# Kernel optimization log

Hardware: AMD Instinct MI355X
Metric: run time of the kernel (lower is better)

The kernel has to match this reference:

```python
import jax, jax.numpy as jnp
import numpy as np

NUM_NODES = 100000
NUM_EDGES = 1200000
IN_CH = 64
HID_CH = 64
NUM_REL = 8
DEG = NUM_EDGES // NUM_NODES  # uniform degree 12


def setup_inputs() -> dict:
    key = jax.random.key(0)
    k1, k2, k3, k4 = jax.random.split(key, 4)
    x = jax.random.normal(k1, (NUM_NODES, IN_CH), dtype=jnp.float32)
    linear = jax.random.normal(k2, (NUM_REL, IN_CH, HID_CH), dtype=jnp.float32) * (1.0 / np.sqrt(IN_CH))
    ptr = jnp.arange(NUM_NODES + 1, dtype=jnp.int64) * DEG  # CSR row pointers, uniform degree
    idx = jax.random.randint(k3, (NUM_EDGES,), 0, NUM_NODES, dtype=jnp.int64)
    edge_types = jax.random.randint(k4, (NUM_EDGES,), 0, NUM_REL, dtype=jnp.int64)
    return {"x": x, "linear": linear, "ptr": ptr, "idx": idx,
            "edge_types": edge_types, "num_node": NUM_NODES}


def reference(x, linear, ptr, idx, edge_types, num_node):
    # Gather source-node features per edge: [E, in]
    gathered = x[idx]
    # Per-edge-type linear transform (loop over small fixed num_rel, like RGCNOP)
    out_e = jnp.zeros((gathered.shape[0], linear.shape[-1]), dtype=gathered.dtype)
    for r in range(linear.shape[0]):
        mask = (edge_types == r).astype(gathered.dtype)[:, None]
        out_e = out_e + mask * (gathered @ linear[r])
    # CSR scatter-sum aggregation over destination segments defined by ptr
    num_edges = idx.shape[0]
    seg_ids = jnp.searchsorted(ptr, jnp.arange(num_edges, dtype=ptr.dtype), side='right') - 1
    agg = jax.ops.segment_sum(out_e, seg_ids, num_segments=num_node)
    # Degree normalization
    deg = (ptr[1:] - ptr[:-1]).astype(agg.dtype)
    return agg / deg[:, None]
```

## Files before the change

kernel.cpp:

```cpp
#include <hip/hip_runtime.h>
#include <hip/hip_bf16.h>


#define THREADS 512
#define NPB 64
#define KDIM 512
#define LDA 520
#define MAXE 1024
#define WFRAG (4 * 16 * 64 * 8)

typedef __attribute__((ext_vector_type(8))) short bf16x8;
typedef __attribute__((ext_vector_type(4))) float f32x4;

extern __shared__ __align__(16) char smem[];

__device__ __forceinline__ unsigned short f2bf(float f) {
  __hip_bfloat16 h = __float2bfloat16(f);
  return *reinterpret_cast<unsigned short*>(&h);
}

__global__ __launch_bounds__(256) void pack_w(const void* __restrict__ wv,
                                              unsigned short* __restrict__ wsB) {
  const int lane = threadIdx.x & 63;
  const unsigned word = ((const unsigned*)wv)[lane];
  const int exf = (int)((word >> 7) & 0xFFu);
  const bool w_bf16 = __popcll(__ballot(exf >= 96 && exf < 160)) >= 48;
  for (int i = blockIdx.x * 256 + threadIdx.x; i < WFRAG; i += gridDim.x * 256) {
    const int j  = i & 7;
    const int l  = (i >> 3) & 63;
    const int kt = (i >> 9) & 15;
    const int nt = i >> 13;
    const int k  = kt * 32 + (l >> 4) * 8 + j;
    const int n  = nt * 16 + (l & 15);
    float v;
    if (w_bf16) v = __bfloat162float(((const __hip_bfloat16*)wv)[k * 64 + n]);
    else        v = ((const float*)wv)[k * 64 + n];
    wsB[i] = f2bf(v);
  }
}

#define ACC_SW(accrow, r, vv)                                        \
  switch (r) {                                                       \
    case 0: accrow[0] += (vv); break; case 1: accrow[1] += (vv); break; \
    case 2: accrow[2] += (vv); break; case 3: accrow[3] += (vv); break; \
    case 4: accrow[4] += (vv); break; case 5: accrow[5] += (vv); break; \
    case 6: accrow[6] += (vv); break; default: accrow[7] += (vv); break; }

__global__ __launch_bounds__(THREADS, 2)
void rgcn_fused(const void* __restrict__ xv,
                const void* __restrict__ wv,
                const int* __restrict__ p32,
                const int* __restrict__ i32,
                const int* __restrict__ t32,
                const unsigned short* __restrict__ wsB,
                float* __restrict__ out,
                int num_nodes) {
  __hip_bfloat16* aggS = (__hip_bfloat16*)smem;
  __hip_bfloat16* wtS  = aggS + NPB * LDA;
  char* tail = smem + (size_t)NPB * LDA * 2 + (wsB ? 0 : (size_t)64 * LDA * 2);
  float*    invS  = (float*)tail;
  int*      ptrS  = (int*)(tail + 256);
  unsigned* eMeta = (unsigned*)(tail + 256 + 272);

  const int tid   = threadIdx.x;
  const int lane  = tid & 63;
  const int wvid  = tid >> 6;
  const int node0 = blockIdx.x * NPB;

  const unsigned xword = ((const unsigned*)xv)[lane];
  const int exf = (int)((xword >> 7) & 0xFFu);
  const bool x_bf16 = __popcll(__ballot(exf >= 96 && exf < 160)) >= 48;
  const bool idx64 = (p32[1] == 0);

  auto ldptr = [&](int n) -> int { return idx64 ? p32[2 * n] : p32[n]; };

  const int ntop   = min(node0 + NPB, num_nodes);
  const int e_lo   = ldptr(node0);
  const int ecount = ldptr(ntop) - e_lo;
  const bool staged = (ecount > 0 && ecount <= MAXE);

  for (int i = tid; i <= NPB; i += THREADS)
    ptrS[i] = ldptr(min(node0 + i, num_nodes));

  if (staged) {
    for (int e = tid; e < ecount; e += THREADS) {
      const int ge = e_lo + e;
      const unsigned s = (unsigned)(idx64 ? i32[2 * ge] : i32[ge]);
      const unsigned r = (unsigned)(idx64 ? t32[2 * ge] : t32[ge]);
      eMeta[e] = s | (r << 24);
    }
  }

  if (!wsB) {
    if (x_bf16) {
      const __hip_bfloat16* wb = (const __hip_bfloat16*)wv;
      for (int i = tid; i < KDIM * 64; i += THREADS)
        wtS[(i & 63) * LDA + (i >> 6)] = wb[i];
    } else {
      const float* wf = (const float*)wv;
      for (int i = tid; i < KDIM * 64; i += THREADS)
        wtS[(i & 63) * LDA + (i >> 6)] = __float2bfloat16(wf[i]);
    }
  }

  __syncthreads();

  for (int i = tid; i < NPB; i += THREADS) {
    const int d = ptrS[i + 1] - ptrS[i];
    invS[i] = (d > 0 && node0 + i < num_nodes) ? 1.0f / (float)d : 0.0f;
  }

  if (staged && tid < NPB) {
    const int e0 = ptrS[tid] - e_lo;
    if (ptrS[tid + 1] - ptrS[tid] == 12) {
      unsigned a[12];
#pragma unroll
      for (int j = 0; j < 12; ++j) a[j] = eMeta[e0 + j];
#pragma unroll
      for (int r = 0; r < 12; ++r)
#pragma unroll
        for (int i = (r & 1); i + 1 < 12; i += 2) {
          const unsigned lo = min(a[i], a[i + 1]);
          const unsigned hi = max(a[i], a[i + 1]);
          a[i] = lo; a[i + 1] = hi;
        }
#pragma unroll
      for (int j = 0; j < 12; ++j) eMeta[e0 + j] = a[j];
    }
  }

  __syncthreads();

  const int c16 = lane & 15;
  const int qd  = lane >> 4;

  auto gather = [&](auto xp, auto loadrow) {
#pragma unroll
    for (int g = 0; g < 2; ++g) {
      const int nlb = wvid * 8 + g * 4;
      const int eq0 = ptrS[nlb + qd] - e_lo;
      const int dq  = ptrS[nlb + qd + 1] - e_lo - eq0;
      const bool okfast = staged && (node0 + nlb + 3 < num_nodes) &&
                          (__ballot(dq == 12) == ~0ull);
      if (okfast) {
        unsigned m[12];
#pragma unroll
        for (int j = 0; j < 12; ++j) m[j] = eMeta[eq0 + j];
        float4 v[12];
#pragma unroll
        for (int j = 0; j < 12; ++j)
          v[j] = loadrow((int)(m[j] & 0x00FFFFFFu), c16);
        __builtin_amdgcn_sched_barrier(0);

        unsigned short* dst0 =
            (unsigned short*)(aggS + (nlb + qd) * LDA) + 4 * c16;
        const ushort4 z4 = {0, 0, 0, 0};
#pragma unroll
        for (int r = 0; r < 8; ++r) *(ushort4*)(dst0 + r * 64) = z4;

        float4 cur = make_float4(0.f, 0.f, 0.f, 0.f);
        unsigned prev = 0xFFFFFFFFu;
#pragma unroll
        for (int j = 0; j < 12; ++j) {
          const unsigned rj = m[j] >> 24;
          const float mk = (rj == prev) ? 1.0f : 0.0f;
          cur.x = fmaf(cur.x, mk, v[j].x);
          cur.y = fmaf(cur.y, mk, v[j].y);
          cur.z = fmaf(cur.z, mk, v[j].z);
          cur.w = fmaf(cur.w, mk, v[j].w);
          ushort4 b;
          b.x = f2bf(cur.x); b.y = f2bf(cur.y);
          b.z = f2bf(cur.z); b.w = f2bf(cur.w);
          *(ushort4*)(dst0 + rj * 64) = b;
          prev = rj;
        }
      } else {
#pragma unroll
        for (int t = 0; t < 4; ++t) {
          const int nl = nlb + t;
          float a[8] = {0.f, 0.f, 0.f, 0.f, 0.f, 0.f, 0.f, 0.f};
          if (node0 + nl < num_nodes) {
            const int e0 = ptrS[nl] - e_lo, e1 = ptrS[nl + 1] - e_lo;
            for (int e = e0; e < e1; ++e) {
              unsigned mm;
              if (staged) mm = eMeta[e];
              else {
                const int ge = e_lo + e;
                mm = (unsigned)(idx64 ? i32[2 * ge] : i32[ge]) |
                     ((unsigned)(idx64 ? t32[2 * ge] : t32[ge]) << 24);
              }
              const float vv = (float)xp[(size_t)(mm & 0x00FFFFFFu) * 64 + lane];
              const int r = __builtin_amdgcn_readfirstlane((int)(mm >> 24));
              ACC_SW(a, r, vv)
            }
          }
#pragma unroll
          for (int r = 0; r < 8; ++r)
            aggS[nl * LDA + r * 64 + lane] = __float2bfloat16(a[r]);
        }
      }
    }
  };

  if (x_bf16) {
    const __hip_bfloat16* xb = (const __hip_bfloat16*)xv;
    auto lr = [&](int src, int c) -> float4 {
      const ushort4 u = ((const ushort4*)xv)[src * 16 + c];
      float4 f;
      f.x = __uint_as_float((unsigned)(unsigned short)u.x << 16);
      f.y = __uint_as_float((unsigned)(unsigned short)u.y << 16);
      f.z = __uint_as_float((unsigned)(unsigned short)u.z << 16);
      f.w = __uint_as_float((unsigned)(unsigned short)u.w << 16);
      return f;
    };
    gather(xb, lr);
  } else {
    const float* xf = (const float*)xv;
    auto lr = [&](int src, int c) -> float4 {
      return ((const float4*)xv)[src * 16 + c];
    };
    gather(xf, lr);
  }

  __syncthreads();

  const int mt  = wvid >> 1;
  const int nt0 = (wvid & 1) * 2;
  const int mi  = lane & 15;
  const int q4  = lane >> 4;
  const __hip_bfloat16* ap = aggS + (mt * 16 + mi) * LDA + q4 * 8;
  f32x4 c0 = {0.f, 0.f, 0.f, 0.f};
  f32x4 c1 = {0.f, 0.f, 0.f, 0.f};
  if (wsB) {
    const bf16x8* B = (const bf16x8*)wsB;
#pragma unroll
    for (int kt = 0; kt < KDIM / 32; ++kt) {
      const bf16x8 a  = *(const bf16x8*)(ap + kt * 32);
      const bf16x8 b0 = B[((nt0 + 0) * 16 + kt) * 64 + lane];
      const bf16x8 b1 = B[((nt0 + 1) * 16 + kt) * 64 + lane];
      c0 = __builtin_amdgcn_mfma_f32_16x16x32_bf16(a, b0, c0, 0, 0, 0);
      c1 = __builtin_amdgcn_mfma_f32_16x16x32_bf16(a, b1, c1, 0, 0, 0);
    }
  } else {
    const __hip_bfloat16* bp0 = wtS + ((nt0 + 0) * 16 + mi) * LDA + q4 * 8;
    const __hip_bfloat16* bp1 = wtS + ((nt0 + 1) * 16 + mi) * LDA + q4 * 8;
#pragma unroll
    for (int kt = 0; kt < KDIM / 32; ++kt) {
      const bf16x8 a  = *(const bf16x8*)(ap  + kt * 32);
      const bf16x8 b0 = *(const bf16x8*)(bp0 + kt * 32);
      const bf16x8 b1 = *(const bf16x8*)(bp1 + kt * 32);
      c0 = __builtin_amdgcn_mfma_f32_16x16x32_bf16(a, b0, c0, 0, 0, 0);
      c1 = __builtin_amdgcn_mfma_f32_16x16x32_bf16(a, b1, c1, 0, 0, 0);
    }
  }

#pragma unroll
  for (int i = 0; i < 4; ++i) {
    const int row  = q4 * 4 + i;
    const int nl   = mt * 16 + row;
    const int node = node0 + nl;
    if (node < num_nodes) {
      const float s = invS[nl];
      out[(size_t)node * 64 + (nt0 + 0) * 16 + mi] = c0[i] * s;
      out[(size_t)node * 64 + (nt0 + 1) * 16 + mi] = c1[i] * s;
    }
  }
}

extern "C" void kernel_launch(void* const* d_in, const int* in_sizes, int n_in,
                              void* d_out, int out_size, void* d_ws, size_t ws_size,
                              hipStream_t stream) {
  const void* x   = d_in[0];
  const void* w   = d_in[1];
  const int*  ptr = (const int*)d_in[2];
  const int*  idx = (const int*)d_in[3];
  const int*  et  = (const int*)d_in[4];
  float*      out = (float*)d_out;

  const int num_nodes = in_sizes[0] / 64;

  const bool useWs = (d_ws != nullptr) &&
                     (ws_size >= (size_t)WFRAG * sizeof(unsigned short));
  unsigned short* wsB = useWs ? (unsigned short*)d_ws : nullptr;
  if (useWs) pack_w<<<32, 256, 0, stream>>>(w, wsB);

  const size_t lds_bytes = (size_t)NPB * LDA * 2 +
                           (useWs ? 0 : (size_t)64 * LDA * 2) +
                           256 + 272 + (size_t)MAXE * 4;

  hipFuncSetAttribute((const void*)rgcn_fused,
                      hipFuncAttributeMaxDynamicSharedMemorySize,
                      (int)lds_bytes);

  const int nblocks = (num_nodes + NPB - 1) / NPB;
  rgcn_fused<<<nblocks, THREADS, lds_bytes, stream>>>(x, w, ptr, idx, et, wsB,
                                                      out, num_nodes);
}
```

Baseline: 138.6 us.

## Pre-convert x to bf16 in workspace and double threads per block

Extends the weight-packing kernel to also convert node features x to a bf16 copy in the workspace. The fused kernel then gathers 8-byte bf16 rows instead of 16-byte fp32 rows, halving random-gather traffic. Block size doubles to 1024 threads so each wave gathers 4 nodes and computes a single 16x16 output tile. The tradeoff is an extra full pass over x (read fp32, write bf16) each call, plus lower occupancy under launch_bounds(1024,2) register limits.

Result: slower. 168.2 us (+21.4%).

```diff
diff --git a/kernel.cpp b/kernel.cpp
--- a/kernel.cpp
+++ b/kernel.cpp
@@ -2,7 +2,7 @@
 #include <hip/hip_bf16.h>
 
 
-#define THREADS 512
+#define THREADS 1024
 #define NPB 64
 #define KDIM 512
 #define LDA 520
@@ -19,23 +19,37 @@
   return *reinterpret_cast<unsigned short*>(&h);
 }
 
-__global__ __launch_bounds__(256) void pack_w(const void* __restrict__ wv,
-                                              unsigned short* __restrict__ wsB) {
+__global__ __launch_bounds__(256) void pack_wx(const void* __restrict__ wv,
+                                               const void* __restrict__ xv,
+                                               unsigned short* __restrict__ wsB,
+                                               unsigned short* __restrict__ wsX,
+                                               int nx) {
   const int lane = threadIdx.x & 63;
-  const unsigned word = ((const unsigned*)wv)[lane];
-  const int exf = (int)((word >> 7) & 0xFFu);
-  const bool w_bf16 = __popcll(__ballot(exf >= 96 && exf < 160)) >= 48;
-  for (int i = blockIdx.x * 256 + threadIdx.x; i < WFRAG; i += gridDim.x * 256) {
-    const int j  = i & 7;
-    const int l  = (i >> 3) & 63;
-    const int kt = (i >> 9) & 15;
-    const int nt = i >> 13;
-    const int k  = kt * 32 + (l >> 4) * 8 + j;
-    const int n  = nt * 16 + (l & 15);
-    float v;
-    if (w_bf16) v = __bfloat162float(((const __hip_bfloat16*)wv)[k * 64 + n]);
-    else        v = ((const float*)wv)[k * 64 + n];
-    wsB[i] = f2bf(v);
+  const unsigned ww = ((const unsigned*)wv)[lane];
+  const int exw = (int)((ww >> 7) & 0xFFu);
+  const bool w_bf16 = __popcll(__ballot(exw >= 96 && exw < 160)) >= 48;
+  const unsigned xw = ((const unsigned*)xv)[lane];
+  const int exx = (int)((xw >> 7) & 0xFFu);
+  const bool x_bf16 = __popcll(__ballot(exx >= 96 && exx < 160)) >= 48;
+
+  const int total = WFRAG + nx;
+  for (int i = blockIdx.x * 256 + threadIdx.x; i < total; i += gridDim.x * 256) {
+    if (i < WFRAG) {
+      const int j  = i & 7;
+      const int l  = (i >> 3) & 63;
+      const int kt = (i >> 9) & 15;
+      const int nt = i >> 13;
+      const int k  = kt * 32 + (l >> 4) * 8 + j;
+      const int n  = nt * 16 + (l & 15);
+      float v;
+      if (w_bf16) v = __bfloat162float(((const __hip_bfloat16*)wv)[k * 64 + n]);
+      else        v = ((const float*)wv)[k * 64 + n];
+      wsB[i] = f2bf(v);
+    } else {
+      const int xi = i - WFRAG;
+      if (x_bf16) wsX[xi] = ((const unsigned short*)xv)[xi];
+      else        wsX[xi] = f2bf(((const float*)xv)[xi]);
+    }
   }
 }
 
@@ -53,6 +67,7 @@
                 const int* __restrict__ i32,
                 const int* __restrict__ t32,
                 const unsigned short* __restrict__ wsB,
+                const unsigned short* __restrict__ wsX,
                 float* __restrict__ out,
                 int num_nodes) {
   __hip_bfloat16* aggS = (__hip_bfloat16*)smem;
@@ -134,76 +149,86 @@
   const int c16 = lane & 15;
   const int qd  = lane >> 4;
 
-  auto gather = [&](auto xp, auto loadrow) {
-#pragma unroll
-    for (int g = 0; g < 2; ++g) {
-      const int nlb = wvid * 8 + g * 4;
-      const int eq0 = ptrS[nlb + qd] - e_lo;
-      const int dq  = ptrS[nlb + qd + 1] - e_lo - eq0;
-      const bool okfast = staged && (node0 + nlb + 3 < num_nodes) &&
-                          (__ballot(dq == 12) == ~0ull);
-      if (okfast) {
-        unsigned m[12];
-#pragma unroll
-        for (int j = 0; j < 12; ++j) m[j] = eMeta[eq0 + j];
-        float4 v[12];
-#pragma unroll
-        for (int j = 0; j < 12; ++j)
-          v[j] = loadrow((int)(m[j] & 0x00FFFFFFu), c16);
-        __builtin_amdgcn_sched_barrier(0);
-
-        unsigned short* dst0 =
-            (unsigned short*)(aggS + (nlb + qd) * LDA) + 4 * c16;
-        const ushort4 z4 = {0, 0, 0, 0};
-#pragma unroll
-        for (int r = 0; r < 8; ++r) *(ushort4*)(dst0 + r * 64) = z4;
-
-        float4 cur = make_float4(0.f, 0.f, 0.f, 0.f);
-        unsigned prev = 0xFFFFFFFFu;
-#pragma unroll
-        for (int j = 0; j < 12; ++j) {
-          const unsigned rj = m[j] >> 24;
-          const float mk = (rj == prev) ? 1.0f : 0.0f;
-          cur.x = fmaf(cur.x, mk, v[j].x);
-          cur.y = fmaf(cur.y, mk, v[j].y);
-          cur.z = fmaf(cur.z, mk, v[j].z);
-          cur.w = fmaf(cur.w, mk, v[j].w);
-          ushort4 b;
-          b.x = f2bf(cur.x); b.y = f2bf(cur.y);
-          b.z = f2bf(cur.z); b.w = f2bf(cur.w);
-          *(ushort4*)(dst0 + rj * 64) = b;
-          prev = rj;
+  auto gather = [&](auto loadrow) {
+    const int nlb = wvid * 4;
+    const int eq0 = ptrS[nlb + qd] - e_lo;
+    const int dq  = ptrS[nlb + qd + 1] - e_lo - eq0;
+    const bool okfast = staged && (node0 + nlb + 3 < num_nodes) &&
+                        (__ballot(dq == 12) == ~0ull);
+    if (okfast) {
+      unsigned m[12];
+#pragma unroll
+      for (int j = 0; j < 12; ++j) m[j] = eMeta[eq0 + j];
+      float4 v[12];
+#pragma unroll
+      for (int j = 0; j < 12; ++j)
+        v[j] = loadrow((int)(m[j] & 0x00FFFFFFu), c16);
+      __builtin_amdgcn_sched_barrier(0);
+
+      unsigned short* dst0 =
+          (unsigned short*)(aggS + (nlb + qd) * LDA) + 4 * c16;
+      const ushort4 z4 = {0, 0, 0, 0};
+#pragma unroll
+      for (int r = 0; r < 8; ++r) *(ushort4*)(dst0 + r * 64) = z4;
+
+      float4 cur = make_float4(0.f, 0.f, 0.f, 0.f);
+      unsigned prev = 0xFFFFFFFFu;
+#pragma unroll
+      for (int j = 0; j < 12; ++j) {
+        const unsigned rj = m[j] >> 24;
+        const float mk = (rj == prev) ? 1.0f : 0.0f;
+        cur.x = fmaf(cur.x, mk, v[j].x);
+        cur.y = fmaf(cur.y, mk, v[j].y);
+        cur.z = fmaf(cur.z, mk, v[j].z);
+        cur.w = fmaf(cur.w, mk, v[j].w);
+        ushort4 b;
+        b.x = f2bf(cur.x); b.y = f2bf(cur.y);
+        b.z = f2bf(cur.z); b.w = f2bf(cur.w);
+        *(ushort4*)(dst0 + rj * 64) = b;
+        prev = rj;
+      }
+    } else {
+#pragma unroll
+      for (int t = 0; t < 4; ++t) {
+        const int nl = nlb + t;
+        float a[8] = {0.f, 0.f, 0.f, 0.f, 0.f, 0.f, 0.f, 0.f};
+        if (node0 + nl < num_nodes) {
+          const int e0 = ptrS[nl] - e_lo, e1 = ptrS[nl + 1] - e_lo;
+          for (int e = e0; e < e1; ++e) {
+            unsigned mm;
+            if (staged) mm = eMeta[e];
+            else {
+              const int ge = e_lo + e;
+              mm = (unsigned)(idx64 ? i32[2 * ge] : i32[ge]) |
+                   ((unsigned)(idx64 ? t32[2 * ge] : t32[ge]) << 24);
+            }
+            const size_t off = (size_t)(mm & 0x00FFFFFFu) * 64 + lane;
+            const float vv = x_bf16
+                ? __bfloat162float(((const __hip_bfloat16*)xv)[off])
+                : ((const float*)xv)[off];
+            const int r = __builtin_amdgcn_readfirstlane((int)(mm >> 24));
+            ACC_SW(a, r, vv)
+          }
         }
-      } else {
-#pragma unroll
-        for (int t = 0; t < 4; ++t) {
-          const int nl = nlb + t;
-          float a[8] = {0.f, 0.f, 0.f, 0.f, 0.f, 0.f, 0.f, 0.f};
-          if (node0 + nl < num_nodes) {
-            const int e0 = ptrS[nl] - e_lo, e1 = ptrS[nl + 1] - e_lo;
-            for (int e = e0; e < e1; ++e) {
-              unsigned mm;
-              if (staged) mm = eMeta[e];
-              else {
-                const int ge = e_lo + e;
-                mm = (unsigned)(idx64 ? i32[2 * ge] : i32[ge]) |
-                     ((unsigned)(idx64 ? t32[2 * ge] : t32[ge]) << 24);
-              }
-              const float vv = (float)xp[(size_t)(mm & 0x00FFFFFFu) * 64 + lane];
-              const int r = __builtin_amdgcn_readfirstlane((int)(mm >> 24));
-              ACC_SW(a, r, vv)
-            }
-          }
-#pragma unroll
-          for (int r = 0; r < 8; ++r)
-            aggS[nl * LDA + r * 64 + lane] = __float2bfloat16(a[r]);
-        }
+#pragma unroll
+        for (int r = 0; r < 8; ++r)
+          aggS[nl * LDA + r * 64 + lane] = __float2bfloat16(a[r]);
       }
     }
   };
 
-  if (x_bf16) {
-    const __hip_bfloat16* xb = (const __hip_bfloat16*)xv;
+  if (wsX) {
+    auto lr = [&](int src, int c) -> float4 {
+      const uint2 u = ((const uint2*)wsX)[src * 16 + c];
+      float4 f;
+      f.x = __uint_as_float(u.x << 16);
+      f.y = __uint_as_float(u.x & 0xFFFF0000u);
+      f.z = __uint_as_float(u.y << 16);
+      f.w = __uint_as_float(u.y & 0xFFFF0000u);
+      return f;
+    };
+    gather(lr);
+  } else if (x_bf16) {
     auto lr = [&](int src, int c) -> float4 {
       const ushort4 u = ((const ushort4*)xv)[src * 16 + c];
       float4 f;
@@ -213,57 +238,46 @@
       f.w = __uint_as_float((unsigned)(unsigned short)u.w << 16);
       return f;
     };
-    gather(xb, lr);
+    gather(lr);
   } else {
-    const float* xf = (const float*)xv;
     auto lr = [&](int src, int c) -> float4 {
       return ((const float4*)xv)[src * 16 + c];
     };
-    gather(xf, lr);
+    gather(lr);
   }
 
   __syncthreads();
 
-  const int mt  = wvid >> 1;
-  const int nt0 = (wvid & 1) * 2;
-  const int mi  = lane & 15;
-  const int q4  = lane >> 4;
+  const int mt = wvid >> 2;
+  const int nt = wvid & 3;
+  const int mi = lane & 15;
+  const int q4 = lane >> 4;
   const __hip_bfloat16* ap = aggS + (mt * 16 + mi) * LDA + q4 * 8;
   f32x4 c0 = {0.f, 0.f, 0.f, 0.f};
-  f32x4 c1 = {0.f, 0.f, 0.f, 0.f};
   if (wsB) {
     const bf16x8* B = (const bf16x8*)wsB;
 #pragma unroll
     for (int kt = 0; kt < KDIM / 32; ++kt) {
-      const bf16x8 a  = *(const bf16x8*)(ap + kt * 32);
-      const bf16x8 b0 = B[((nt0 + 0) * 16 + kt) * 64 + lane];
-      const bf16x8 b1 = B[((nt0 + 1) * 16 + kt) * 64 + lane];
-      c0 = __builtin_amdgcn_mfma_f32_16x16x32_bf16(a, b0, c0, 0, 0, 0);
-      c1 = __builtin_amdgcn_mfma_f32_16x16x32_bf16(a, b1, c1, 0, 0, 0);
+      const bf16x8 a = *(const bf16x8*)(ap + kt * 32);
+      const bf16x8 b = B[(nt * 16 + kt) * 64 + lane];
+      c0 = __builtin_amdgcn_mfma_f32_16x16x32_bf16(a, b, c0, 0, 0, 0);
     }
   } else {
-    const __hip_bfloat16* bp0 = wtS + ((nt0 + 0) * 16 + mi) * LDA + q4 * 8;
-    const __hip_bfloat16* bp1 = wtS + ((nt0 + 1) * 16 + mi) * LDA + q4 * 8;
+    const __hip_bfloat16* bp = wtS + (nt * 16 + mi) * LDA + q4 * 8;
 #pragma unroll
     for (int kt = 0; kt < KDIM / 32; ++kt) {
-      const bf16x8 a  = *(const bf16x8*)(ap  + kt * 32);
-      const bf16x8 b0 = *(const bf16x8*)(bp0 + kt * 32);
-      const bf16x8 b1 = *(const bf16x8*)(bp1 + kt * 32);
-      c0 = __builtin_amdgcn_mfma_f32_16x16x32_bf16(a, b0, c0, 0, 0, 0);
-      c1 = __builtin_amdgcn_mfma_f32_16x16x32_bf16(a, b1, c1, 0, 0, 0);
+      const bf16x8 a = *(const bf16x8*)(ap + kt * 32);
+      const bf16x8 b = *(const bf16x8*)(bp + kt * 32);
+      c0 = __builtin_amdgcn_mfma_f32_16x16x32_bf16(a, b, c0, 0, 0, 0);
     }
   }
 
 #pragma unroll
   for (int i = 0; i < 4; ++i) {
-    const int row  = q4 * 4 + i;
-    const int nl   = mt * 16 + row;
+    const int nl   = mt * 16 + q4 * 4 + i;
     const int node = node0 + nl;
-    if (node < num_nodes) {
-      const float s = invS[nl];
-      out[(size_t)node * 64 + (nt0 + 0) * 16 + mi] = c0[i] * s;
-      out[(size_t)node * 64 + (nt0 + 1) * 16 + mi] = c1[i] * s;
-    }
+    if (node < num_nodes)
+      out[(size_t)node * 64 + nt * 16 + mi] = c0[i] * invS[nl];
   }
 }
 
@@ -278,14 +292,20 @@
   float*      out = (float*)d_out;
 
   const int num_nodes = in_sizes[0] / 64;
-
-  const bool useWs = (d_ws != nullptr) &&
-                     (ws_size >= (size_t)WFRAG * sizeof(unsigned short));
-  unsigned short* wsB = useWs ? (unsigned short*)d_ws : nullptr;
-  if (useWs) pack_w<<<32, 256, 0, stream>>>(w, wsB);
+  const int nx = num_nodes * 64;
+
+  const size_t needB = (size_t)WFRAG * 2;
+  const size_t needX = needB + (size_t)nx * 2;
+  const bool haveB = (d_ws != nullptr) && (ws_size >= needB);
+  const bool haveX = (d_ws != nullptr) && (ws_size >= needX);
+  unsigned short* wsB = haveB ? (unsigned short*)d_ws : nullptr;
+  unsigned short* wsX = haveX ? (unsigned short*)d_ws + WFRAG : nullptr;
+
+  if (haveB)
+    pack_wx<<<256, 256, 0, stream>>>(w, x, wsB, wsX, haveX ? nx : 0);
 
   const size_t lds_bytes = (size_t)NPB * LDA * 2 +
-                           (useWs ? 0 : (size_t)64 * LDA * 2) +
+                           (haveB ? 0 : (size_t)64 * LDA * 2) +
                            256 + 272 + (size_t)MAXE * 4;
 
   hipFuncSetAttribute((const void*)rgcn_fused,
@@ -294,5 +314,5 @@
 
   const int nblocks = (num_nodes + NPB - 1) / NPB;
   rgcn_fused<<<nblocks, THREADS, lds_bytes, stream>>>(x, w, ptr, idx, et, wsB,
-                                                      out, num_nodes);
+                                                      wsX, out, num_nodes);
 }
```

## Prepack x to bf16 and sorted edge metadata in a pre-pass kernel

Applied to the files above, without the earlier changes.

A combined pre-pass kernel packs W into MFMA fragments, converts x to a bf16 copy in workspace, narrows ptr to int32, and builds per-node sorted packed (src|type) edge metadata. The fused kernel then reads the precomputed metadata and bf16 rows directly, so it no longer stages and sorts edges in LDS or needs the barriers around that. This halves gather bytes, and the lower LDS use lets occupancy rise to 4 blocks per CU. In exchange, the pre-pass adds a full read and write of x plus the edge arrays, and one more launch each call.

After: 143.7 us. 3.7% more time.

```diff
diff --git a/kernel.cpp b/kernel.cpp
--- a/kernel.cpp
+++ b/kernel.cpp
@@ -6,7 +6,6 @@
 #define NPB 64
 #define KDIM 512
 #define LDA 520
-#define MAXE 1024
 #define WFRAG (4 * 16 * 64 * 8)
 
 typedef __attribute__((ext_vector_type(8))) short bf16x8;
@@ -19,13 +18,37 @@
   return *reinterpret_cast<unsigned short*>(&h);
 }
 
-__global__ __launch_bounds__(256) void pack_w(const void* __restrict__ wv,
-                                              unsigned short* __restrict__ wsB) {
+#define ACC_SW(accrow, r, vv)                                        \
+  switch (r) {                                                       \
+    case 0: accrow[0] += (vv); break; case 1: accrow[1] += (vv); break; \
+    case 2: accrow[2] += (vv); break; case 3: accrow[3] += (vv); break; \
+    case 4: accrow[4] += (vv); break; case 5: accrow[5] += (vv); break; \
+    case 6: accrow[6] += (vv); break; default: accrow[7] += (vv); break; }
+
+__global__ __launch_bounds__(256)
+void pack_all(const void* __restrict__ wv, const void* __restrict__ xv,
+              const int* __restrict__ p32, const int* __restrict__ i32,
+              const int* __restrict__ t32,
+              unsigned short* __restrict__ wsB,
+              unsigned short* __restrict__ wsX,
+              int* __restrict__ ptr32, unsigned* __restrict__ mPack,
+              int nx, int nnodes) {
   const int lane = threadIdx.x & 63;
-  const unsigned word = ((const unsigned*)wv)[lane];
-  const int exf = (int)((word >> 7) & 0xFFu);
-  const bool w_bf16 = __popcll(__ballot(exf >= 96 && exf < 160)) >= 48;
-  for (int i = blockIdx.x * 256 + threadIdx.x; i < WFRAG; i += gridDim.x * 256) {
+  const unsigned ww = ((const unsigned*)wv)[lane];
+  const int exw = (int)((ww >> 7) & 0xFFu);
+  const bool w_bf16 = __popcll(__ballot(exw >= 96 && exw < 160)) >= 48;
+  const unsigned xw = ((const unsigned*)xv)[lane];
+  const int exx = (int)((xw >> 7) & 0xFFu);
+  const bool x_bf16 = __popcll(__ballot(exx >= 96 && exx < 160)) >= 48;
+  const bool idx64 = (p32[1] == 0);
+
+  const int tW = wsB ? WFRAG : 0;
+  const int tX = wsX ? (nx + 7) / 8 : 0;
+  const int tN = (ptr32 && mPack) ? (nnodes + 1) : 0;
+
+  int gid = blockIdx.x * 256 + threadIdx.x;
+  if (gid < tW) {
+    const int i = gid;
     const int j  = i & 7;
     const int l  = (i >> 3) & 63;
     const int kt = (i >> 9) & 15;
@@ -36,31 +59,84 @@
     if (w_bf16) v = __bfloat162float(((const __hip_bfloat16*)wv)[k * 64 + n]);
     else        v = ((const float*)wv)[k * 64 + n];
     wsB[i] = f2bf(v);
+    return;
+  }
+  gid -= tW;
+  if (gid < tX) {
+    const int base = gid * 8;
+    if (base + 8 <= nx) {
+      if (x_bf16) {
+        *(uint4*)(wsX + base) = *(const uint4*)((const unsigned short*)xv + base);
+      } else {
+        const float4 a = *(const float4*)((const float*)xv + base);
+        const float4 b = *(const float4*)((const float*)xv + base + 4);
+        ushort4 lo, hi;
+        lo.x = f2bf(a.x); lo.y = f2bf(a.y); lo.z = f2bf(a.z); lo.w = f2bf(a.w);
+        hi.x = f2bf(b.x); hi.y = f2bf(b.y); hi.z = f2bf(b.z); hi.w = f2bf(b.w);
+        *(ushort4*)(wsX + base)     = lo;
+        *(ushort4*)(wsX + base + 4) = hi;
+      }
+    } else {
+      for (int i = base; i < nx; ++i)
+        wsX[i] = x_bf16 ? ((const unsigned short*)xv)[i]
+                        : f2bf(((const float*)xv)[i]);
+    }
+    return;
+  }
+  gid -= tX;
+  if (gid < tN) {
+    const int n = gid;
+    const int pn = idx64 ? p32[2 * n] : p32[n];
+    ptr32[n] = pn;
+    if (n < nnodes) {
+      const int e1 = idx64 ? p32[2 * n + 2] : p32[n + 1];
+      const int deg = e1 - pn;
+      if (deg == 12) {
+        unsigned a[12];
+#pragma unroll
+        for (int j = 0; j < 12; ++j) {
+          const int e = pn + j;
+          const unsigned s = (unsigned)(idx64 ? i32[2 * e] : i32[e]);
+          const unsigned r = (unsigned)(idx64 ? t32[2 * e] : t32[e]);
+          a[j] = s | (r << 24);
+        }
+#pragma unroll
+        for (int rr = 0; rr < 12; ++rr)
+#pragma unroll
+          for (int i = (rr & 1); i + 1 < 12; i += 2) {
+            const unsigned lo = min(a[i], a[i + 1]);
+            const unsigned hi = max(a[i], a[i + 1]);
+            a[i] = lo; a[i + 1] = hi;
+          }
+#pragma unroll
+        for (int j = 0; j < 12; ++j) mPack[pn + j] = a[j];
+      } else {
+        for (int e = pn; e < e1; ++e) {
+          const unsigned s = (unsigned)(idx64 ? i32[2 * e] : i32[e]);
+          const unsigned r = (unsigned)(idx64 ? t32[2 * e] : t32[e]);
+          mPack[e] = s | (r << 24);
+        }
+      }
+    }
   }
 }
 
-#define ACC_SW(accrow, r, vv)                                        \
-  switch (r) {                                                       \
-    case 0: accrow[0] += (vv); break; case 1: accrow[1] += (vv); break; \
-    case 2: accrow[2] += (vv); break; case 3: accrow[3] += (vv); break; \
-    case 4: accrow[4] += (vv); break; case 5: accrow[5] += (vv); break; \
-    case 6: accrow[6] += (vv); break; default: accrow[7] += (vv); break; }
-
-__global__ __launch_bounds__(THREADS, 2)
+__global__ __launch_bounds__(THREADS, 4)
 void rgcn_fused(const void* __restrict__ xv,
                 const void* __restrict__ wv,
                 const int* __restrict__ p32,
                 const int* __restrict__ i32,
                 const int* __restrict__ t32,
                 const unsigned short* __restrict__ wsB,
+                const unsigned short* __restrict__ wsX,
+                const int* __restrict__ ptr32,
+                const unsigned* __restrict__ mPack,
                 float* __restrict__ out,
                 int num_nodes) {
   __hip_bfloat16* aggS = (__hip_bfloat16*)smem;
   __hip_bfloat16* wtS  = aggS + NPB * LDA;
-  char* tail = smem + (size_t)NPB * LDA * 2 + (wsB ? 0 : (size_t)64 * LDA * 2);
-  float*    invS  = (float*)tail;
-  int*      ptrS  = (int*)(tail + 256);
-  unsigned* eMeta = (unsigned*)(tail + 256 + 272);
+  float* invS = (float*)(smem + (size_t)NPB * LDA * 2 +
+                         (wsB ? 0 : (size_t)64 * LDA * 2));
 
   const int tid   = threadIdx.x;
   const int lane  = tid & 63;
@@ -71,25 +147,7 @@
   const int exf = (int)((xword >> 7) & 0xFFu);
   const bool x_bf16 = __popcll(__ballot(exf >= 96 && exf < 160)) >= 48;
   const bool idx64 = (p32[1] == 0);
-
-  auto ldptr = [&](int n) -> int { return idx64 ? p32[2 * n] : p32[n]; };
-
-  const int ntop   = min(node0 + NPB, num_nodes);
-  const int e_lo   = ldptr(node0);
-  const int ecount = ldptr(ntop) - e_lo;
-  const bool staged = (ecount > 0 && ecount <= MAXE);
-
-  for (int i = tid; i <= NPB; i += THREADS)
-    ptrS[i] = ldptr(min(node0 + i, num_nodes));
-
-  if (staged) {
-    for (int e = tid; e < ecount; e += THREADS) {
-      const int ge = e_lo + e;
-      const unsigned s = (unsigned)(idx64 ? i32[2 * ge] : i32[ge]);
-      const unsigned r = (unsigned)(idx64 ? t32[2 * ge] : t32[ge]);
-      eMeta[e] = s | (r << 24);
-    }
-  }
+  const bool direct = (mPack != nullptr);
 
   if (!wsB) {
     if (x_bf16) {
@@ -103,123 +161,107 @@
     }
   }
 
-  __syncthreads();
-
-  for (int i = tid; i < NPB; i += THREADS) {
-    const int d = ptrS[i + 1] - ptrS[i];
-    invS[i] = (d > 0 && node0 + i < num_nodes) ? 1.0f / (float)d : 0.0f;
-  }
-
-  if (staged && tid < NPB) {
-    const int e0 = ptrS[tid] - e_lo;
-    if (ptrS[tid + 1] - ptrS[tid] == 12) {
-      unsigned a[12];
-#pragma unroll
-      for (int j = 0; j < 12; ++j) a[j] = eMeta[e0 + j];
-#pragma unroll
-      for (int r = 0; r < 12; ++r)
-#pragma unroll
-        for (int i = (r & 1); i + 1 < 12; i += 2) {
-          const unsigned lo = min(a[i], a[i + 1]);
-          const unsigned hi = max(a[i], a[i + 1]);
-          a[i] = lo; a[i + 1] = hi;
-        }
-#pragma unroll
-      for (int j = 0; j < 12; ++j) eMeta[e0 + j] = a[j];
-    }
-  }
-
-  __syncthreads();
-
   const int c16 = lane & 15;
   const int qd  = lane >> 4;
 
-  auto gather = [&](auto xp, auto loadrow) {
-#pragma unroll
-    for (int g = 0; g < 2; ++g) {
-      const int nlb = wvid * 8 + g * 4;
-      const int eq0 = ptrS[nlb + qd] - e_lo;
-      const int dq  = ptrS[nlb + qd + 1] - e_lo - eq0;
-      const bool okfast = staged && (node0 + nlb + 3 < num_nodes) &&
-                          (__ballot(dq == 12) == ~0ull);
-      if (okfast) {
-        unsigned m[12];
-#pragma unroll
-        for (int j = 0; j < 12; ++j) m[j] = eMeta[eq0 + j];
-        float4 v[12];
-#pragma unroll
-        for (int j = 0; j < 12; ++j)
-          v[j] = loadrow((int)(m[j] & 0x00FFFFFFu), c16);
-        __builtin_amdgcn_sched_barrier(0);
-
-        unsigned short* dst0 =
-            (unsigned short*)(aggS + (nlb + qd) * LDA) + 4 * c16;
-        const ushort4 z4 = {0, 0, 0, 0};
-#pragma unroll
-        for (int r = 0; r < 8; ++r) *(ushort4*)(dst0 + r * 64) = z4;
-
-        float4 cur = make_float4(0.f, 0.f, 0.f, 0.f);
-        unsigned prev = 0xFFFFFFFFu;
-#pragma unroll
-        for (int j = 0; j < 12; ++j) {
-          const unsigned rj = m[j] >> 24;
-          const float mk = (rj == prev) ? 1.0f : 0.0f;
-          cur.x = fmaf(cur.x, mk, v[j].x);
-          cur.y = fmaf(cur.y, mk, v[j].y);
-          cur.z = fmaf(cur.z, mk, v[j].z);
-          cur.w = fmaf(cur.w, mk, v[j].w);
-          ushort4 b;
-          b.x = f2bf(cur.x); b.y = f2bf(cur.y);
-          b.z = f2bf(cur.z); b.w = f2bf(cur.w);
-          *(ushort4*)(dst0 + rj * 64) = b;
-          prev = rj;
+  auto flushAcc = [&](int nl, const unsigned* m, const uint2* u) {
+    unsigned short* dst0 = (unsigned short*)(aggS + nl * LDA) + 4 * c16;
+    const ushort4 z4 = {0, 0, 0, 0};
+#pragma unroll
+    for (int r = 0; r < 8; ++r) *(ushort4*)(dst0 + r * 64) = z4;
+    float4 cur = make_float4(0.f, 0.f, 0.f, 0.f);
+    unsigned prev = 0xFFFFFFFFu;
+#pragma unroll
+    for (int j = 0; j < 12; ++j) {
+      const unsigned rj = m[j] >> 24;
+      const float mk = (rj == prev) ? 1.0f : 0.0f;
+      cur.x = fmaf(cur.x, mk, __uint_as_float(u[j].x << 16));
+      cur.y = fmaf(cur.y, mk, __uint_as_float(u[j].x & 0xFFFF0000u));
+      cur.z = fmaf(cur.z, mk, __uint_as_float(u[j].y << 16));
+      cur.w = fmaf(cur.w, mk, __uint_as_float(u[j].y & 0xFFFF0000u));
+      ushort4 bb;
+      bb.x = f2bf(cur.x); bb.y = f2bf(cur.y);
+      bb.z = f2bf(cur.z); bb.w = f2bf(cur.w);
+      *(ushort4*)(dst0 + rj * 64) = bb;
+      prev = rj;
+    }
+  };
+
+  auto genericGroup = [&](int nlb) {
+#pragma unroll
+    for (int t = 0; t < 4; ++t) {
+      const int nl = nlb + t;
+      const int node = node0 + nl;
+      float a[8] = {0.f, 0.f, 0.f, 0.f, 0.f, 0.f, 0.f, 0.f};
+      int d = 0;
+      if (node < num_nodes) {
+        int e0, e1;
+        if (direct) { e0 = ptr32[node]; e1 = ptr32[node + 1]; }
+        else {
+          e0 = idx64 ? p32[2 * node]     : p32[node];
+          e1 = idx64 ? p32[2 * node + 2] : p32[node + 1];
         }
-      } else {
-#pragma unroll
-        for (int t = 0; t < 4; ++t) {
-          const int nl = nlb + t;
-          float a[8] = {0.f, 0.f, 0.f, 0.f, 0.f, 0.f, 0.f, 0.f};
-          if (node0 + nl < num_nodes) {
-            const int e0 = ptrS[nl] - e_lo, e1 = ptrS[nl + 1] - e_lo;
-            for (int e = e0; e < e1; ++e) {
-              unsigned mm;
-              if (staged) mm = eMeta[e];
-              else {
-                const int ge = e_lo + e;
-                mm = (unsigned)(idx64 ? i32[2 * ge] : i32[ge]) |
-                     ((unsigned)(idx64 ? t32[2 * ge] : t32[ge]) << 24);
-              }
-              const float vv = (float)xp[(size_t)(mm & 0x00FFFFFFu) * 64 + lane];
-              const int r = __builtin_amdgcn_readfirstlane((int)(mm >> 24));
-              ACC_SW(a, r, vv)
-            }
+        d = e1 - e0;
+        for (int e = e0; e < e1; ++e) {
+          unsigned mm;
+          if (direct) mm = mPack[e];
+          else
+            mm = (unsigned)(idx64 ? i32[2 * e] : i32[e]) |
+                 ((unsigned)(idx64 ? t32[2 * e] : t32[e]) << 24);
+          const size_t off = (size_t)(mm & 0x00FFFFFFu) * 64 + lane;
+          float vv;
+          if (wsX) {
+            vv = __uint_as_float((unsigned)wsX[off] << 16);
+          } else {
+            vv = x_bf16 ? __bfloat162float(((const __hip_bfloat16*)xv)[off])
+                        : ((const float*)xv)[off];
           }
-#pragma unroll
-          for (int r = 0; r < 8; ++r)
-            aggS[nl * LDA + r * 64 + lane] = __float2bfloat16(a[r]);
+          const int r = __builtin_amdgcn_readfirstlane((int)(mm >> 24));
+          ACC_SW(a, r, vv)
         }
       }
+#pragma unroll
+      for (int r = 0; r < 8; ++r)
+        aggS[nl * LDA + r * 64 + lane] = __float2bfloat16(a[r]);
+      if (lane == 0)
+        invS[nl] = (d > 0 && node < num_nodes) ? 1.0f / (float)d : 0.0f;
     }
   };
 
-  if (x_bf16) {
-    const __hip_bfloat16* xb = (const __hip_bfloat16*)xv;
-    auto lr = [&](int src, int c) -> float4 {
-      const ushort4 u = ((const ushort4*)xv)[src * 16 + c];
-      float4 f;
-      f.x = __uint_as_float((unsigned)(unsigned short)u.x << 16);
-      f.y = __uint_as_float((unsigned)(unsigned short)u.y << 16);
-      f.z = __uint_as_float((unsigned)(unsigned short)u.z << 16);
-      f.w = __uint_as_float((unsigned)(unsigned short)u.w << 16);
-      return f;
-    };
-    gather(xb, lr);
-  } else {
-    const float* xf = (const float*)xv;
-    auto lr = [&](int src, int c) -> float4 {
-      return ((const float4*)xv)[src * 16 + c];
-    };
-    gather(xf, lr);
+  bool done = false;
+  if (direct && wsX) {
+    const int nlA = wvid * 8 + qd;
+    const int nlB = nlA + 4;
+    const int nodeA = node0 + nlA, nodeB = node0 + nlB;
+    int e0A = 0, dA = 0, e0B = 0, dB = 0;
+    if (nodeA < num_nodes) { e0A = ptr32[nodeA]; dA = ptr32[nodeA + 1] - e0A; }
+    if (nodeB < num_nodes) { e0B = ptr32[nodeB]; dB = ptr32[nodeB + 1] - e0B; }
+    if (__ballot(dA == 12 && dB == 12) == ~0ull) {
+      unsigned mA[12], mB[12];
+#pragma unroll
+      for (int j = 0; j < 12; ++j) mA[j] = mPack[e0A + j];
+#pragma unroll
+      for (int j = 0; j < 12; ++j) mB[j] = mPack[e0B + j];
+      uint2 uA[12], uB[12];
+#pragma unroll
+      for (int j = 0; j < 12; ++j)
+        uA[j] = ((const uint2*)wsX)[(size_t)(mA[j] & 0x00FFFFFFu) * 16 + c16];
+#pragma unroll
+      for (int j = 0; j < 12; ++j)
+        uB[j] = ((const uint2*)wsX)[(size_t)(mB[j] & 0x00FFFFFFu) * 16 + c16];
+      __builtin_amdgcn_sched_barrier(0);
+      flushAcc(nlA, mA, uA);
+      flushAcc(nlB, mB, uB);
+      if (c16 == 0) {
+        invS[nlA] = 1.0f / 12.0f;
+        invS[nlB] = 1.0f / 12.0f;
+      }
+      done = true;
+    }
+  }
+  if (!done) {
+    genericGroup(wvid * 8);
+    genericGroup(wvid * 8 + 4);
   }
 
   __syncthreads();
@@ -256,8 +298,7 @@
 
 #pragma unroll
   for (int i = 0; i < 4; ++i) {
-    const int row  = q4 * 4 + i;
-    const int nl   = mt * 16 + row;
+    const int nl   = mt * 16 + q4 * 4 + i;
     const int node = node0 + nl;
     if (node < num_nodes) {
       const float s = invS[nl];
@@ -278,15 +319,39 @@
   float*      out = (float*)d_out;
 
   const int num_nodes = in_sizes[0] / 64;
-
-  const bool useWs = (d_ws != nullptr) &&
-                     (ws_size >= (size_t)WFRAG * sizeof(unsigned short));
-  unsigned short* wsB = useWs ? (unsigned short*)d_ws : nullptr;
-  if (useWs) pack_w<<<32, 256, 0, stream>>>(w, wsB);
+  const int nx = num_nodes * 64;
+  const int E  = in_sizes[3];
+
+  const size_t offB = 0, szB = (size_t)WFRAG * 2;
+  const size_t offM = offB + szB, szM = (size_t)E * 4;
+  const size_t offP = (offM + szM + 15) & ~(size_t)15;
+  const size_t szP  = (size_t)(num_nodes + 1) * 4;
+  const size_t offX = (offP + szP + 15) & ~(size_t)15;
+  const size_t szX  = (size_t)nx * 2;
+
+  const bool haveB = d_ws && ws_size >= offB + szB;
+  const bool haveM = d_ws && ws_size >= offP + szP;
+  const bool haveX = d_ws && ws_size >= offX + szX;
+
+  char* wsc = (char*)d_ws;
+  unsigned short* wsB  = haveB ? (unsigned short*)(wsc + offB) : nullptr;
+  unsigned*       mP   = haveM ? (unsigned*)(wsc + offM)       : nullptr;
+  int*            pt32 = haveM ? (int*)(wsc + offP)            : nullptr;
+  unsigned short* wsX  = haveX ? (unsigned short*)(wsc + offX) : nullptr;
+
+  const long long tW = haveB ? WFRAG : 0;
+  const long long tX = haveX ? (nx + 7) / 8 : 0;
+  const long long tN = haveM ? (num_nodes + 1) : 0;
+  const long long total = tW + tX + tN;
+  if (total > 0) {
+    const int pblocks = (int)((total + 255) / 256);
+    pack_all<<<pblocks, 256, 0, stream>>>(w, x, ptr, idx, et, wsB, wsX,
+                                          pt32, mP, nx, num_nodes);
+  }
 
   const size_t lds_bytes = (size_t)NPB * LDA * 2 +
-                           (useWs ? 0 : (size_t)64 * LDA * 2) +
-                           256 + 272 + (size_t)MAXE * 4;
+                           (haveB ? 0 : (size_t)64 * LDA * 2) +
+                           (size_t)NPB * sizeof(float);
 
   hipFuncSetAttribute((const void*)rgcn_fused,
                       hipFuncAttributeMaxDynamicSharedMemorySize,
@@ -294,5 +359,6 @@
 
   const int nblocks = (num_nodes + NPB - 1) / NPB;
   rgcn_fused<<<nblocks, THREADS, lds_bytes, stream>>>(x, w, ptr, idx, et, wsB,
-                                                      out, num_nodes);
+                                                      wsX, pt32, mP, out,
+                                                      num_nodes);
 }
```
